# Performance work log

Measured on AMD Instinct MI355X. Metric: run time of the kernel, lower is better.

The kernel has to match this reference:

```python
import jax, jax.numpy as jnp
import numpy as np

B, N, E, D, L = 64, 128, 2048, 128, 4  # graphs, nodes/graph, edges/graph, channels, gnn layers
T = B * N  # total batched nodes


def setup_inputs() -> dict:
    key = jax.random.key(0)
    ks = jax.random.split(key, 16)
    s = 1.0 / np.sqrt(D)
    sc = 1.0 / np.sqrt(2 * D)
    inp = {
        "x": jax.random.normal(ks[0], (B, N, D), jnp.float32),
        "edges": jax.random.randint(ks[1], (B, 2, E), 0, N, dtype=jnp.int32),
        "Wg": jax.random.normal(ks[2], (L, D, D), jnp.float32) * s,
        "bg": jnp.zeros((L, D), jnp.float32),
        "Wq": jax.random.normal(ks[3], (D, D), jnp.float32) * s,
        "bq": jnp.zeros((D,), jnp.float32),
        "Wk": jax.random.normal(ks[4], (D, D), jnp.float32) * s,
        "bk": jnp.zeros((D,), jnp.float32),
        "Wv": jax.random.normal(ks[5], (D, D), jnp.float32) * s,
        "bv": jnp.zeros((D,), jnp.float32),
        "Wo": jax.random.normal(ks[6], (D, D), jnp.float32) * s,
        "bo": jnp.zeros((D,), jnp.float32),
        "Wc": jax.random.normal(ks[7], (2 * D, D), jnp.float32) * sc,
        "bc": jnp.zeros((D,), jnp.float32),
    }
    return inp


def _batched_edges(edges):
    # offset per-graph edge indices into the flat [T] node space, add self-loops
    off = (jnp.arange(B, dtype=edges.dtype) * N)[:, None]
    src = (edges[:, 0, :] + off).reshape(-1)
    dst = (edges[:, 1, :] + off).reshape(-1)
    loops = jnp.arange(T, dtype=edges.dtype)
    src = jnp.concatenate([src, loops])
    dst = jnp.concatenate([dst, loops])
    return src, dst


def reference(x, edges, Wg, bg, Wq, bq, Wk, bk, Wv, bv, Wo, bo, Wc, bc):
    xf = x.reshape(T, D)  # flat batched node features (torch_geo_batch.x)
    src, dst = _batched_edges(edges)
    # GCN symmetric normalization with self-loops: deg >= 1
    deg = jax.ops.segment_sum(jnp.ones(src.shape, xf.dtype), dst, num_segments=T)
    norm = jax.lax.rsqrt(deg)
    coef = (norm[src] * norm[dst])[:, None]
    # n_layers of GCNConv + tanh
    h = xf
    for l in range(L):
        m = h @ Wg[l]  # [T, D]
        h = jax.ops.segment_sum(m[src] * coef, dst, num_segments=T) + bg[l]
        h = jnp.tanh(h)
    batch_embedding = h.reshape(B, N, D)
    # DoubleHeadedAttention on the ORIGINAL batched input x; both inputs are
    # identical so the two attention heads compute the same tensor.
    q = xf @ Wq + bq
    k = xf @ Wk + bk
    v = xf @ Wv + bv
    attn = jax.nn.softmax(q @ k.T, axis=-1)  # [T, T]
    attended = (attn @ v) @ Wo + bo  # output_layer, == attended_input1 == attended_input2
    combined = jnp.concatenate([attended, attended], axis=-1)  # [T, 2D]
    att_output = combined @ Wc + bc  # combination_layer
    return jnp.concatenate([batch_embedding, att_output.reshape(B, N, D)], axis=-1)
```

## Files before the change

kernel.cpp:

```cpp
#include <hip/hip_runtime.h>
#include <math.h>

#define TT 8192
#define DD 128
#define GB 64
#define GN 128
#define GE 2048

#define WS_WG16    0u
#define WS_W2      (644u<<10)
#define WS_B2      (708u<<10)
#define WS_Q16     (1u<<20)
#define WS_K16     (3u<<20)
#define WS_VT      (5u<<20)
#define WS_OPART   (7u<<20)
#define WS_PM8     (23u<<20)
#define WS_PL8     ((23u<<20)+(256u<<10))
#define WS_PM16    (39u<<20)
#define WS_PL16    ((39u<<20)+(512u<<10))
#define WS_NEED16  (41u<<20)

typedef _Float16 hfrag  __attribute__((ext_vector_type(8)));
typedef _Float16 h4     __attribute__((ext_vector_type(4)));
typedef float    ffrag  __attribute__((ext_vector_type(4)));

#define MFMA16(a,b,c) __builtin_amdgcn_mfma_f32_16x16x32_f16((a),(b),(c),0,0,0)

typedef __attribute__((address_space(1))) unsigned int gu32_t;
typedef __attribute__((address_space(3))) unsigned int lu32_t;
#define GLOAD16(gp, lp) __builtin_amdgcn_global_load_lds((gu32_t*)(const void*)(gp), (lu32_t*)(void*)(lp), 16, 0, 0)

__device__ __forceinline__ int fidx(int r_, int c_) {
  return (((r_>>4)*4 + (c_>>5))*64 + (r_&15) + 16*((c_>>3)&3))*8 + (c_&7);
}

__device__ __forceinline__ float tanh_fast(float x) {
  float e = __expf(2.f*x);
  return 1.f - 2.f/(e+1.f);
}

__global__ __launch_bounds__(512) void k_prep(const float* __restrict__ Wg,
                                              const float* __restrict__ Wo, const float* __restrict__ bo,
                                              const float* __restrict__ Wc, const float* __restrict__ bc,
                                              _Float16* __restrict__ wg16,
                                              float* __restrict__ W2, float* __restrict__ b2) {
  __shared__ float Wcs[128*128];
  const int tid = threadIdx.x;
  const int bid = blockIdx.x;
  if (bid < 4) {
    #pragma unroll
    for (int i=0;i<32;++i){
      int i2 = i*512 + tid;
      Wcs[i2] = Wc[i2] + Wc[i2 + 16384];
    }
    __syncthreads();
    const int r  = tid>>4;
    const int c0 = (tid&15)*8;
    const int ig = bid*32 + r;
    float acc[8];
    #pragma unroll
    for (int m=0;m<8;++m) acc[m]=0.f;
    for (int k=0;k<128;++k){
      float wo = Wo[ig*DD + k];
      #pragma unroll
      for (int m=0;m<8;++m) acc[m] += wo*Wcs[k*128 + c0 + m];
    }
    #pragma unroll
    for (int m=0;m<8;++m) W2[ig*DD + c0 + m] = acc[m];
    if (bid == 0){
      __syncthreads();
      if (tid < 128){
        float s = bc[tid];
        for (int k=0;k<128;++k) s += bo[k]*Wcs[k*128 + tid];
        b2[tid] = s;
      }
    }
  } else {
    const int l = bid - 4;
    const float* Wl = Wg + l*DD*DD;
    _Float16* dst = wg16 + l*16384;
    #pragma unroll
    for (int i=0;i<8;++i){
      int i4 = i*512 + tid;
      int k = i4>>5, i0 = (i4&31)<<2;
      float4 v = *(const float4*)&Wl[k*DD + i0];
      dst[fidx(i0+0,k)] = (_Float16)v.x;
      dst[fidx(i0+1,k)] = (_Float16)v.y;
      dst[fidx(i0+2,k)] = (_Float16)v.z;
      dst[fidx(i0+3,k)] = (_Float16)v.w;
    }
  }
}

__global__ __launch_bounds__(512,1) void fused_pre(
    const float* __restrict__ x, const int* __restrict__ edges,
    const _Float16* __restrict__ wg16, const float* __restrict__ bg,
    const float* __restrict__ Wq, const float* __restrict__ bq_,
    const float* __restrict__ Wk, const float* __restrict__ bk_,
    const float* __restrict__ Wv, const float* __restrict__ bv_,
    _Float16* __restrict__ q16, _Float16* __restrict__ k16, _Float16* __restrict__ vT,
    float* __restrict__ out)
{
  __shared__ __align__(16) char Lm[135168];
  const int tid  = threadIdx.x;
  const int bid  = blockIdx.x;

  if (bid < 64) {
    float*    Af   = (float*)Lm;
    _Float16* W16f = (_Float16*)Lm;
    _Float16* m16  = (_Float16*)(Lm + 32768);
    _Float16* h16  = (_Float16*)(Lm + 65536);
    _Float16* A16  = (_Float16*)(Lm + 98304);
    int*      cnt  = (int*)(Lm + 131072);
    float*    nrm  = (float*)(Lm + 131584);

    const int lane = tid & 63;
    const int w8   = tid >> 6;
    const int l15  = lane & 15;
    const int g    = lane >> 4;
    const int wi   = w8 >> 2;
    const int wj   = w8 & 3;
    const int b    = bid;
    const int* eg  = edges + b*2*GE;

    #pragma unroll
    for (int i=0;i<8;++i) ((float4*)Af)[i*512 + tid] = (float4){0.f,0.f,0.f,0.f};
    if (tid < 128) cnt[tid] = 0;
    __syncthreads();
    #pragma unroll
    for (int i=0;i<4;++i) atomicAdd(&cnt[eg[GE + i*512 + tid]], 1);
    __syncthreads();
    if (tid < 128) nrm[tid] = rsqrtf(1.f + (float)cnt[tid]);
    __syncthreads();
    #pragma unroll
    for (int i=0;i<4;++i){
      int s = eg[i*512 + tid], d = eg[GE + i*512 + tid];
      atomicAdd(&Af[d*128 + s], nrm[s]*nrm[d]);
    }
    __syncthreads();
    if (tid < 128) Af[tid*128 + tid] += nrm[tid]*nrm[tid];
    __syncthreads();
    #pragma unroll
    for (int i=0;i<8;++i){
      int i4 = i*512 + tid;
      float4 v = ((const float4*)Af)[i4];
      int dst = i4>>5, s4 = (i4&31)<<2;
      h4 t; t[0]=(_Float16)v.x; t[1]=(_Float16)v.y; t[2]=(_Float16)v.z; t[3]=(_Float16)v.w;
      *(h4*)&A16[fidx(dst, s4)] = t;
    }
    #pragma unroll
    for (int i=0;i<8;++i){
      int i4 = i*512 + tid;
      int n = i4>>5, k4 = (i4&31)<<2;
      float4 v = *(const float4*)&x[((size_t)b*128 + n)*128 + k4];
      h4 t; t[0]=(_Float16)v.x; t[1]=(_Float16)v.y; t[2]=(_Float16)v.z; t[3]=(_Float16)v.w;
      *(h4*)&h16[fidx(n, k4)] = t;
    }
    __syncthreads();
    #pragma unroll
    for (int i=0;i<4;++i){
      const int c = i*8 + w8;
      GLOAD16(wg16 + c*512 + lane*8, &W16f[c*512]);
    }
    asm volatile("s_waitcnt vmcnt(0)" ::: "memory");
    __syncthreads();

    for (int l=0; l<4; ++l){
      {
        hfrag bf[2][4];
        #pragma unroll
        for (int jj=0;jj<2;++jj){
          const int jg = wj*2+jj;
          #pragma unroll
          for (int ds=0;ds<4;++ds) bf[jj][ds] = *(const hfrag*)&h16[(jg*4+ds)*512 + lane*8];
        }
        #pragma unroll
        for (int it=0;it<4;++it){
          const int Ri = wi*4+it;
          hfrag af[4];
          #pragma unroll
          for (int ds=0;ds<4;++ds) af[ds] = *(const hfrag*)&W16f[(Ri*4+ds)*512 + lane*8];
          #pragma unroll
          for (int jj=0;jj<2;++jj){
            ffrag acc = (ffrag){0.f,0.f,0.f,0.f};
            #pragma unroll
            for (int ds=0;ds<4;++ds) acc = MFMA16(af[ds], bf[jj][ds], acc);
            const int src = (wj*2+jj)*16 + l15;
            const int sds = src>>5, s16 = 16*((src>>3)&3), s7 = src&7;
            #pragma unroll
            for (int r=0;r<4;++r)
              m16[((Ri*4 + sds)*64 + 4*g + r + s16)*8 + s7] = (_Float16)acc[r];
          }
        }
      }
      __syncthreads();
      if (l < 3){
        #pragma unroll
        for (int i=0;i<4;++i){
          const int c = i*8 + w8;
          GLOAD16(wg16 + (l+1)*16384 + c*512 + lane*8, &W16f[c*512]);
        }
      }
      {
        hfrag bf[2][4];
        float bgv[2];
        #pragma unroll
        for (int jj=0;jj<2;++jj){
          const int jg = wj*2+jj;
          #pragma unroll
          for (int ds=0;ds<4;++ds) bf[jj][ds] = *(const hfrag*)&m16[(jg*4+ds)*512 + lane*8];
          bgv[jj] = bg[l*DD + jg*16 + l15];
        }
        #pragma unroll
        for (int it=0;it<4;++it){
          const int Ri = wi*4+it;
          hfrag af[4];
          #pragma unroll
          for (int ds=0;ds<4;++ds) af[ds] = *(const hfrag*)&A16[(Ri*4+ds)*512 + lane*8];
          #pragma unroll
          for (int jj=0;jj<2;++jj){
            ffrag acc = (ffrag){0.f,0.f,0.f,0.f};
            #pragma unroll
            for (int ds=0;ds<4;++ds) acc = MFMA16(af[ds], bf[jj][ds], acc);
            const int dout = (wj*2+jj)*16 + l15;
            if (l < 3){
              const int dds = dout>>5, d16 = 16*((dout>>3)&3), d7 = dout&7;
              #pragma unroll
              for (int r=0;r<4;++r){
                float v = tanh_fast(acc[r] + bgv[jj]);
                h16[((Ri*4 + dds)*64 + 4*g + r + d16)*8 + d7] = (_Float16)v;
              }
            } else {
              #pragma unroll
              for (int r=0;r<4;++r){
                float v = tanh_fast(acc[r] + bgv[jj]);
                out[((size_t)b*128 + Ri*16 + 4*g + r)*(2*DD) + dout] = v;
              }
            }
          }
        }
      }
      __syncthreads();
    }
  } else {
    const int idx  = bid - 64;
    const int mode = idx >> 6;
    const int row0 = (idx & 63) * 128;
    const float* W    = (mode==0) ? Wq : (mode==1) ? Wk : Wv;
    const float* bias = (mode==0) ? bq_ : (mode==1) ? bk_ : bv_;
    float* Xs  = (float*)Lm;
    float* Ws2 = (float*)(Lm + 67584);

    #pragma unroll
    for (int i=0;i<8;++i){
      int i2 = i*512 + tid;
      int r = i2>>5, c4 = (i2&31)<<2;
      *(float4*)&Ws2[r*132+c4] = *(const float4*)&W[r*DD + c4];
      *(float4*)&Xs [r*132+c4] = *(const float4*)&x[(size_t)(row0+r)*DD + c4];
    }
    __syncthreads();

    const int r0 = (tid>>4)*4;
    const int cg = tid&15;
    const int c0 = cg*8;
    float acc[4][8];
    #pragma unroll
    for (int t=0;t<4;++t)
      #pragma unroll
      for (int m=0;m<8;++m) acc[t][m]=0.f;
    for (int kk=0;kk<128;kk+=4){
      float a[4][4];
      #pragma unroll
      for (int t=0;t<4;++t) *(float4*)a[t] = *(float4*)&Xs[(r0+t)*132+kk];
      #pragma unroll
      for (int j=0;j<4;++j){
        float w[8];
        *(float4*)&w[0] = *(float4*)&Ws2[(kk+j)*132+c0];
        *(float4*)&w[4] = *(float4*)&Ws2[(kk+j)*132+c0+4];
        #pragma unroll
        for (int t=0;t<4;++t)
          #pragma unroll
          for (int m=0;m<8;++m) acc[t][m] += a[t][j]*w[m];
      }
    }
    #pragma unroll
    for (int t=0;t<4;++t){
      const int row = row0 + r0 + t;
      float val[8];
      #pragma unroll
      for (int m=0;m<8;++m) val[m] = acc[t][m] + bias[c0+m];
      if (mode == 0) {
        hfrag h;
        #pragma unroll
        for (int m=0;m<8;++m) h[m] = (_Float16)val[m];
        *(hfrag*)&q16[(size_t)row*DD + c0] = h;
      } else if (mode == 1) {
        hfrag h;
        #pragma unroll
        for (int m=0;m<8;++m) h[m] = (_Float16)val[m];
        int R = row>>4, l15r = row&15, dsx = cg>>2, gx = cg&3;
        *(hfrag*)&k16[((size_t)(R*4+dsx)*64 + l15r + 16*gx)*8] = h;
      } else {
        int C = row>>5, kloc = row&31;
        int gx = (kloc&15)>>2;
        int jx = ((kloc>>4)<<2) | (kloc&3);
        #pragma unroll
        for (int m=0;m<8;++m){
          int d = c0+m;
          vT[((size_t)(C*8 + (d>>4))*64 + (d&15) + 16*gx)*8 + jx] = (_Float16)val[m];
        }
      }
    }
  }
}

template<int KS>
__global__ __launch_bounds__(512,2) void k_flash(
    const _Float16* __restrict__ q16, const _Float16* __restrict__ k16f,
    const _Float16* __restrict__ vTf,
    _Float16* __restrict__ Opart, float* __restrict__ pm, float* __restrict__ pl)
{
  constexpr int SLICE = TT/KS;
  constexpr int NT    = SLICE/64;
  __shared__ _Float16 Kb[2][8192];
  __shared__ _Float16 Vb[2][8192];
  const int tid  = threadIdx.x;
  const int lane = tid & 63;
  const int w8   = tid >> 6;
  const int l15  = lane & 15;
  const int g    = lane >> 4;
  const int qt   = blockIdx.x / KS;
  const int sp   = blockIdx.x % KS;
  const int q0   = qt*256 + w8*32;

  hfrag qf[2][4];
  #pragma unroll
  for (int qb=0;qb<2;++qb)
    #pragma unroll
    for (int ds=0;ds<4;++ds)
      qf[qb][ds] = *(const hfrag*)&q16[(size_t)(q0+16*qb+l15)*DD + 32*ds + 8*g];

  float mrun[2] = {-1e30f,-1e30f}, lrun[2] = {0.f,0.f};
  ffrag o[2][8];
  #pragma unroll
  for (int qb=0;qb<2;++qb)
    #pragma unroll
    for (int nt=0;nt<8;++nt) o[qb][nt] = (ffrag){0.f,0.f,0.f,0.f};

  const size_t kbase = (size_t)(sp*SLICE)*DD;
  {
    const _Float16* Ks = k16f + kbase;
    const _Float16* Vs = vTf  + kbase;
    #pragma unroll
    for (int j=0;j<2;++j){
      const int c = w8*2 + j;
      GLOAD16(Ks + c*512 + lane*8, &Kb[0][c*512]);
      GLOAD16(Vs + c*512 + lane*8, &Vb[0][c*512]);
    }
  }
  __syncthreads();

  int cur = 0;
  for (int t=0; t<NT; ++t){
    if (t < NT-1){
      const _Float16* Ks = k16f + kbase + (size_t)(t+1)*64*DD;
      const _Float16* Vs = vTf  + kbase + (size_t)(t+1)*64*DD;
      #pragma unroll
      for (int j=0;j<2;++j){
        const int c = w8*2 + j;
        GLOAD16(Ks + c*512 + lane*8, &Kb[cur^1][c*512]);
        GLOAD16(Vs + c*512 + lane*8, &Vb[cur^1][c*512]);
      }
    }

    ffrag s2[2][4];
    #pragma unroll
    for (int qb=0;qb<2;++qb)
      #pragma unroll
      for (int mt=0;mt<4;++mt) s2[qb][mt] = (ffrag){0.f,0.f,0.f,0.f};
    __builtin_amdgcn_s_setprio(1);
    #pragma unroll
    for (int mt=0;mt<4;++mt)
      #pragma unroll
      for (int ds=0;ds<4;++ds){
        hfrag kf = *(const hfrag*)&Kb[cur][(mt*4+ds)*512 + lane*8];
        s2[0][mt] = MFMA16(kf, qf[0][ds], s2[0][mt]);
        s2[1][mt] = MFMA16(kf, qf[1][ds], s2[1][mt]);
      }
    __builtin_amdgcn_s_setprio(0);

    #pragma unroll
    for (int qb=0;qb<2;++qb){
      float tmax = -1e30f;
      #pragma unroll
      for (int mt=0;mt<4;++mt)
        tmax = fmaxf(tmax, fmaxf(fmaxf(s2[qb][mt][0], s2[qb][mt][1]),
                                 fmaxf(s2[qb][mt][2], s2[qb][mt][3])));
      tmax = fmaxf(tmax, __shfl_xor(tmax,16));
      tmax = fmaxf(tmax, __shfl_xor(tmax,32));
      const float mnew = fmaxf(mrun[qb], tmax);
      float psum = 0.f;
      #pragma unroll
      for (int mt=0;mt<4;++mt)
        #pragma unroll
        for (int r=0;r<4;++r){ float e = __expf(s2[qb][mt][r]-mnew); s2[qb][mt][r]=e; psum += e; }
      psum += __shfl_xor(psum,16);
      psum += __shfl_xor(psum,32);
      if (__any(mnew > mrun[qb])){
        const float sc = __expf(mrun[qb]-mnew);
        lrun[qb] = lrun[qb]*sc + psum;
        mrun[qb] = mnew;
        #pragma unroll
        for (int r=0;r<4;++r){
          const float scr = __shfl(sc, 4*g+r);
          #pragma unroll
          for (int nt=0;nt<8;++nt) o[qb][nt][r] *= scr;
        }
      } else {
        lrun[qb] += psum;
      }
    }

    __builtin_amdgcn_s_setprio(1);
    #pragma unroll
    for (int c2=0;c2<2;++c2){
      hfrag pf0, pf1;
      #pragma unroll
      for (int j=0;j<8;++j){
        pf0[j] = (_Float16)s2[0][2*c2+(j>>2)][j&3];
        pf1[j] = (_Float16)s2[1][2*c2+(j>>2)][j&3];
      }
      #pragma unroll
      for (int nt=0;nt<8;++nt){
        hfrag vf = *(const hfrag*)&Vb[cur][(c2*8+nt)*512 + lane*8];
        o[0][nt] = MFMA16(pf0, vf, o[0][nt]);
        o[1][nt] = MFMA16(pf1, vf, o[1][nt]);
      }
    }
    __builtin_amdgcn_s_setprio(0);

    __syncthreads();
    cur ^= 1;
  }

  #pragma unroll
  for (int qb=0;qb<2;++qb){
    #pragma unroll
    for (int r=0;r<4;++r){
      _Float16* dst = &Opart[((size_t)sp*TT + q0 + 16*qb + 4*g + r)*DD];
      #pragma unroll
      for (int nt=0;nt<8;++nt)
        dst[16*nt + l15] = (_Float16)o[qb][nt][r];
    }
    if (g==0){
      pm[(size_t)sp*TT + q0 + 16*qb + l15] = mrun[qb];
      pl[(size_t)sp*TT + q0 + 16*qb + l15] = lrun[qb];
    }
  }
}

template<int NS>
__global__ __launch_bounds__(256) void k_gemm_final(const _Float16* __restrict__ Opart,
                                                    const float* __restrict__ pm, const float* __restrict__ pl,
                                                    const float* __restrict__ W2, const float* __restrict__ b2,
                                                    float* __restrict__ out) {
  __shared__ float As[32*132];
  __shared__ float Ws[128*132];
  int tid = threadIdx.x;
  int row0 = blockIdx.x*32;
  #pragma unroll
  for (int i=0;i<4;i++){
    int idx = i*256+tid;
    int r = idx>>5, c4 = (idx&31)<<2;
    int t = row0 + r;
    float ms[NS], ls[NS];
    #pragma unroll
    for (int s=0;s<NS;++s){ ms[s]=pm[(size_t)s*TT+t]; ls[s]=pl[(size_t)s*TT+t]; }
    float mx = ms[0];
    #pragma unroll
    for (int s=1;s<NS;++s) mx = fmaxf(mx, ms[s]);
    float es[NS]; float den = 0.f;
    #pragma unroll
    for (int s=0;s<NS;++s){ es[s]=__expf(ms[s]-mx); den += ls[s]*es[s]; }
    float4 vv = {0.f,0.f,0.f,0.f};
    #pragma unroll
    for (int s=0;s<NS;++s){
      float us = es[s]/den;
      h4 a = *(const h4*)&Opart[((size_t)s*TT + t)*DD + c4];
      vv.x += us*(float)a[0]; vv.y += us*(float)a[1];
      vv.z += us*(float)a[2]; vv.w += us*(float)a[3];
    }
    *(float4*)&As[r*132+c4] = vv;
  }
  #pragma unroll
  for (int i=0;i<16;i++){
    int idx = i*256+tid;
    int r = idx>>5, c4 = (idx&31)<<2;
    *(float4*)&Ws[r*132+c4] = *(const float4*)&W2[r*DD + c4];
  }
  __syncthreads();
  int rg = tid>>4, cg = tid&15;
  int r0 = rg*2, c0 = cg*8;
  float acc[2][8];
  #pragma unroll
  for (int a=0;a<2;a++)
    #pragma unroll
    for (int b=0;b<8;b++) acc[a][b]=0.f;
  for (int kk=0;kk<128;kk+=4){
    float a0[4], a1[4];
    *(float4*)a0 = *(float4*)&As[r0*132+kk];
    *(float4*)a1 = *(float4*)&As[(r0+1)*132+kk];
    #pragma unroll
    for (int j=0;j<4;j++){
      float w[8];
      *(float4*)&w[0] = *(float4*)&Ws[(kk+j)*132+c0];
      *(float4*)&w[4] = *(float4*)&Ws[(kk+j)*132+c0+4];
      #pragma unroll
      for (int m=0;m<8;m++){
        acc[0][m] += a0[j]*w[m];
        acc[1][m] += a1[j]*w[m];
      }
    }
  }
  #pragma unroll
  for (int a=0;a<2;a++){
    float outv[8];
    #pragma unroll
    for (int m=0;m<8;m++) outv[m] = acc[a][m] + b2[c0+m];
    float* dst = &out[(size_t)(row0+r0+a)*(2*DD) + DD + c0];
    *(float4*)&dst[0] = *(float4*)&outv[0];
    *(float4*)&dst[4] = *(float4*)&outv[4];
  }
}

extern "C" void kernel_launch(void* const* d_in, const int* in_sizes, int n_in,
                              void* d_out, int out_size, void* d_ws, size_t ws_size,
                              hipStream_t stream) {
  const float* x  = (const float*)d_in[0];
  const int* edges = (const int*)d_in[1];
  const float* Wg = (const float*)d_in[2];
  const float* bg = (const float*)d_in[3];
  const float* Wq = (const float*)d_in[4];
  const float* bq = (const float*)d_in[5];
  const float* Wk = (const float*)d_in[6];
  const float* bk = (const float*)d_in[7];
  const float* Wv = (const float*)d_in[8];
  const float* bv = (const float*)d_in[9];
  const float* Wo = (const float*)d_in[10];
  const float* bo = (const float*)d_in[11];
  const float* Wc = (const float*)d_in[12];
  const float* bc = (const float*)d_in[13];
  float* out = (float*)d_out;
  char* ws = (char*)d_ws;

  _Float16* wg16 = (_Float16*)(ws + WS_WG16);
  float* W2  = (float*)(ws + WS_W2);
  float* b2  = (float*)(ws + WS_B2);
  _Float16* Opart = (_Float16*)(ws + WS_OPART);
  _Float16* q16 = (_Float16*)(ws + WS_Q16);
  _Float16* k16 = (_Float16*)(ws + WS_K16);
  _Float16* vT  = (_Float16*)(ws + WS_VT);

  k_prep<<<8,512,0,stream>>>(Wg, Wo, bo, Wc, bc, wg16, W2, b2);
  fused_pre<<<256,512,0,stream>>>(x, edges, wg16, bg, Wq, bq, Wk, bk, Wv, bv,
                                  q16, k16, vT, out);

  if (ws_size >= WS_NEED16) {
    float* pm = (float*)(ws + WS_PM16);
    float* pl = (float*)(ws + WS_PL16);
    k_flash<16><<<512,512,0,stream>>>(q16, k16, vT, Opart, pm, pl);
    k_gemm_final<16><<<256,256,0,stream>>>(Opart, pm, pl, W2, b2, out);
  } else {
    float* pm = (float*)(ws + WS_PM8);
    float* pl = (float*)(ws + WS_PL8);
    k_flash<8><<<256,512,0,stream>>>(q16, k16, vT, Opart, pm, pl);
    k_gemm_final<8><<<256,256,0,stream>>>(Opart, pm, pl, W2, b2, out);
  }
}
```

Measured before the change: 114.2 us.

## Add 1024-thread flash kernel sharing each K/V tile across 512 queries

```diff
diff --git a/kernel.cpp b/kernel.cpp
--- a/kernel.cpp
+++ b/kernel.cpp
@@ -314,6 +314,140 @@
   }
 }
 
+__global__ __launch_bounds__(1024,4) void k_flash6(
+    const _Float16* __restrict__ q16, const _Float16* __restrict__ k16f,
+    const _Float16* __restrict__ vTf,
+    _Float16* __restrict__ Opart, float* __restrict__ pm, float* __restrict__ pl)
+{
+  constexpr int KS = 16;
+  constexpr int SLICE = TT/KS;
+  constexpr int NT = SLICE/64;
+  __shared__ _Float16 Kb[2][8192];
+  __shared__ _Float16 Vb[2][8192];
+  const int tid  = threadIdx.x;
+  const int lane = tid & 63;
+  const int w16  = tid >> 6;
+  const int l15  = lane & 15;
+  const int g    = lane >> 4;
+  const int qt   = blockIdx.x >> 4;
+  const int sp   = blockIdx.x & 15;
+  const int q0   = qt*512 + w16*32;
+
+  hfrag qf[2][4];
+  #pragma unroll
+  for (int qb=0;qb<2;++qb)
+    #pragma unroll
+    for (int ds=0;ds<4;++ds)
+      qf[qb][ds] = *(const hfrag*)&q16[(size_t)(q0+16*qb+l15)*DD + 32*ds + 8*g];
+
+  float mrun[2] = {-1e30f,-1e30f}, lrun[2] = {0.f,0.f};
+  ffrag o[2][8];
+  #pragma unroll
+  for (int qb=0;qb<2;++qb)
+    #pragma unroll
+    for (int nt=0;nt<8;++nt) o[qb][nt] = (ffrag){0.f,0.f,0.f,0.f};
+
+  const size_t kbase = (size_t)(sp*SLICE)*DD;
+  {
+    GLOAD16(k16f + kbase + w16*512 + lane*8, &Kb[0][w16*512]);
+    GLOAD16(vTf  + kbase + w16*512 + lane*8, &Vb[0][w16*512]);
+  }
+  __syncthreads();
+
+  int cur = 0;
+  for (int t=0; t<NT; ++t){
+    if (t < NT-1){
+      const size_t nb = kbase + (size_t)(t+1)*64*DD;
+      GLOAD16(k16f + nb + w16*512 + lane*8, &Kb[cur^1][w16*512]);
+      GLOAD16(vTf  + nb + w16*512 + lane*8, &Vb[cur^1][w16*512]);
+    }
+
+    ffrag s2[2][4];
+    #pragma unroll
+    for (int qb=0;qb<2;++qb)
+      #pragma unroll
+      for (int mt=0;mt<4;++mt) s2[qb][mt] = (ffrag){0.f,0.f,0.f,0.f};
+    __builtin_amdgcn_s_setprio(1);
+    #pragma unroll
+    for (int mt=0;mt<4;++mt)
+      #pragma unroll
+      for (int ds=0;ds<4;++ds){
+        hfrag kf = *(const hfrag*)&Kb[cur][(mt*4+ds)*512 + lane*8];
+        s2[0][mt] = MFMA16(kf, qf[0][ds], s2[0][mt]);
+        s2[1][mt] = MFMA16(kf, qf[1][ds], s2[1][mt]);
+      }
+    __builtin_amdgcn_s_setprio(0);
+
+    #pragma unroll
+    for (int qb=0;qb<2;++qb){
+      float tmax = -1e30f;
+      #pragma unroll
+      for (int mt=0;mt<4;++mt)
+        tmax = fmaxf(tmax, fmaxf(fmaxf(s2[qb][mt][0], s2[qb][mt][1]),
+                                 fmaxf(s2[qb][mt][2], s2[qb][mt][3])));
+      tmax = fmaxf(tmax, __shfl_xor(tmax,16));
+      tmax = fmaxf(tmax, __shfl_xor(tmax,32));
+      const float mnew = fmaxf(mrun[qb], tmax);
+      float psum = 0.f;
+      #pragma unroll
+      for (int mt=0;mt<4;++mt)
+        #pragma unroll
+        for (int r=0;r<4;++r){ float e = __expf(s2[qb][mt][r]-mnew); s2[qb][mt][r]=e; psum += e; }
+      psum += __shfl_xor(psum,16);
+      psum += __shfl_xor(psum,32);
+      if (__any(mnew > mrun[qb])){
+        const float sc = __expf(mrun[qb]-mnew);
+        lrun[qb] = lrun[qb]*sc + psum;
+        mrun[qb] = mnew;
+        #pragma unroll
+        for (int r=0;r<4;++r){
+          const float scr = __shfl(sc, 4*g+r);
+          #pragma unroll
+          for (int nt=0;nt<8;++nt) o[qb][nt][r] *= scr;
+        }
+      } else {
+        lrun[qb] += psum;
+      }
+    }
+
+    __builtin_amdgcn_s_setprio(1);
+    #pragma unroll
+    for (int c2=0;c2<2;++c2){
+      hfrag pf0, pf1;
+      #pragma unroll
+      for (int j=0;j<8;++j){
+        pf0[j] = (_Float16)s2[0][2*c2+(j>>2)][j&3];
+        pf1[j] = (_Float16)s2[1][2*c2+(j>>2)][j&3];
+      }
+      #pragma unroll
+      for (int nt=0;nt<8;++nt){
+        hfrag vf = *(const hfrag*)&Vb[cur][(c2*8+nt)*512 + lane*8];
+        o[0][nt] = MFMA16(pf0, vf, o[0][nt]);
+        o[1][nt] = MFMA16(pf1, vf, o[1][nt]);
+      }
+    }
+    __builtin_amdgcn_s_setprio(0);
+
+    __syncthreads();
+    cur ^= 1;
+  }
+
+  #pragma unroll
+  for (int qb=0;qb<2;++qb){
+    #pragma unroll
+    for (int r=0;r<4;++r){
+      _Float16* dst = &Opart[((size_t)sp*TT + q0 + 16*qb + 4*g + r)*DD];
+      #pragma unroll
+      for (int nt=0;nt<8;++nt)
+        dst[16*nt + l15] = (_Float16)o[qb][nt][r];
+    }
+    if (g==0){
+      pm[(size_t)sp*TT + q0 + 16*qb + l15] = mrun[qb];
+      pl[(size_t)sp*TT + q0 + 16*qb + l15] = lrun[qb];
+    }
+  }
+}
+
 template<int KS>
 __global__ __launch_bounds__(512,2) void k_flash(
     const _Float16* __restrict__ q16, const _Float16* __restrict__ k16f,
@@ -568,7 +702,7 @@
   if (ws_size >= WS_NEED16) {
     float* pm = (float*)(ws + WS_PM16);
     float* pl = (float*)(ws + WS_PL16);
-    k_flash<16><<<512,512,0,stream>>>(q16, k16, vT, Opart, pm, pl);
+    k_flash6<<<256,1024,0,stream>>>(q16, k16, vT, Opart, pm, pl);
     k_gemm_final<16><<<256,256,0,stream>>>(Opart, pm, pl, W2, b2, out);
   } else {
     float* pm = (float*)(ws + WS_PM8);
```

Result: slower. 173.4 us (+51.8%).
